# Performance work log

Hardware: AMD Instinct MI355X
Metric: run time of the kernel (lower is better)

## Reference

```python
import jax, jax.numpy as jnp
import numpy as np

NUM_ITERATIONS = 3  # matches init kwarg num_iterations
B, R, CIN, COUT, K = 32, 2048, 64, 64, 16


def squash(s):
    # squash along the last (capsule-vector) axis, as in the torch module
    sq = jnp.sum(s * s, axis=-1, keepdims=True)
    return (sq / (1.0 + sq)) * s / jnp.sqrt(sq)


def setup_inputs() -> dict:
    key = jax.random.key(0)
    k1, k2 = jax.random.split(key)
    x = jax.random.normal(k1, (B, R, CIN), dtype=jnp.float32)
    route_weights = jax.random.normal(k2, (K, R, CIN, COUT), dtype=jnp.float32) * 0.05
    return {"x": x, "route_weights": route_weights}


def reference(x, route_weights):
    # priors[k,b,r,o] = sum_c x[b,r,c] * W[k,r,c,o]   -> [K, B, R, COUT]
    priors = jnp.einsum('brc,krco->kbro', x, route_weights)
    logits = jnp.zeros(priors.shape[:3] + (1,), dtype=priors.dtype)  # [K,B,R,1]
    outputs = None
    for i in range(NUM_ITERATIONS):
        probs = jax.nn.softmax(logits, axis=2)  # softmax over route nodes (torch dim=2)
        outputs = squash(jnp.sum(probs * priors, axis=2, keepdims=True))  # [K,B,1,COUT]
        if i != NUM_ITERATIONS - 1:
            logits = logits + jnp.sum(priors * outputs, axis=-1, keepdims=True)
    return outputs[:, :, 0, :]  # [K, B, COUT]
```

## Files before the change

### kernel.cpp

```cpp
#include <hip/hip_runtime.h>
#include <hip/hip_bf16.h>
#include <stdint.h>

#define NB 32
#define NR 2048
#define NC 64
#define NO 64
#define NK 16

using bf16x8 = __attribute__((ext_vector_type(8))) short;
using f32x4  = __attribute__((ext_vector_type(4))) float;

__device__ __forceinline__ uint32_t f2bf(float f) {
  uint32_t u = __builtin_bit_cast(uint32_t, f);
  return (u + 0x7fffu + ((u >> 16) & 1u)) >> 16;
}
__device__ __forceinline__ uint32_t packbf2(float lo, float hi) {
  return f2bf(lo) | (f2bf(hi) << 16);
}
__device__ __forceinline__ uint32_t cvtpk2(float lo, float hi) {
  float2 v; v.x = lo; v.y = hi;
  __hip_bfloat162 h = __float22bfloat162_rn(v);
  uint32_t r;
  __builtin_memcpy(&r, &h, 4);
  return r;
}

__device__ __forceinline__ void gload_lds16(const float* g, float* l) {
  __builtin_amdgcn_global_load_lds(
      (const __attribute__((address_space(1))) void*)g,
      (__attribute__((address_space(3))) void*)l, 16, 0, 0);
}

__global__ __launch_bounds__(256) void make_xbf(const float* __restrict__ x,
                                                ushort* __restrict__ xbf) {
  __shared__ float tile[32][72];
  const int r = blockIdx.x, t = threadIdx.x;
  {
    const int b = t >> 3, c0 = (t & 7) << 3;
    const float* xp = x + ((size_t)b * NR + r) * NC + c0;
    *(float4*)&tile[b][c0] = *(const float4*)xp;
    *(float4*)&tile[b][c0 + 4] = *(const float4*)(xp + 4);
  }
  __syncthreads();
  {
    const int ks = t >> 7, mt = (t >> 6) & 1, l = t & 63;
    const int b = mt * 16 + (l & 15);
    const int cb = ks * 32 + (l >> 4) * 8;
    uint4 uv;
    uv.x = packbf2(tile[b][cb + 0], tile[b][cb + 1]);
    uv.y = packbf2(tile[b][cb + 2], tile[b][cb + 3]);
    uv.z = packbf2(tile[b][cb + 4], tile[b][cb + 5]);
    uv.w = packbf2(tile[b][cb + 6], tile[b][cb + 7]);
    *(uint4*)(xbf + (size_t)r * 2048 + t * 8) = uv;
  }
}

__global__ __launch_bounds__(256, 2) void priors_gemm(const ushort* __restrict__ xbf,
                                                      const float* __restrict__ W,
                                                      ushort* __restrict__ priors) {
  __shared__ float ldsW[2][4][2048];
  const int w = threadIdx.x >> 6, lane = threadIdx.x & 63;
  const int g = lane >> 4, col = lane & 15;
  const int kq = blockIdx.x & 3, rblk = blockIdx.x >> 2;
  const int k = kq * 4 + w;

  f32x4 acc[2][4];

  auto stage = [&](int rr, int ks, int buf) {
    const float* srcrow = W + ((size_t)(k * NR + rblk * 8 + rr)) * 4096 + ks * 2048;
    float* dst = &ldsW[buf][w][0] + lane * 4;
    const int j = lane & 15;
#pragma unroll
    for (int i = 0; i < 8; ++i) {
      const int c = i * 4 + (lane >> 4);
      const int gc = c >> 3;
      const int jj = j ^ (gc & 3) ^ ((gc >> 1) << 2);
      gload_lds16(srcrow + c * 64 + jj * 4, dst + i * 256);
    }
  };

  auto compute = [&](int rr, int ks, int buf) {
    const float* pw = &ldsW[buf][w][0];
    const size_t r = rblk * 8 + rr;
    bf16x8 af0 = *(const bf16x8*)(xbf + ((r * 2 + ks) * 2 + 0) * 512 + lane * 8);
    bf16x8 af1 = *(const bf16x8*)(xbf + ((r * 2 + ks) * 2 + 1) * 512 + lane * 8);
#pragma unroll
    for (int nt = 0; nt < 4; ++nt) {
      const int oo = (nt * 16 + col) ^ ((g & 3) << 2) ^ ((g >> 1) << 4);
      float f[8];
#pragma unroll
      for (int e = 0; e < 8; ++e) f[e] = pw[(g * 8 + e) * 64 + oo];
      uint4 uv;
      uv.x = cvtpk2(f[0], f[1]);
      uv.y = cvtpk2(f[2], f[3]);
      uv.z = cvtpk2(f[4], f[5]);
      uv.w = cvtpk2(f[6], f[7]);
      bf16x8 bfr = __builtin_bit_cast(bf16x8, uv);
      acc[0][nt] = __builtin_amdgcn_mfma_f32_16x16x32_bf16(af0, bfr, acc[0][nt], 0, 0, 0);
      acc[1][nt] = __builtin_amdgcn_mfma_f32_16x16x32_bf16(af1, bfr, acc[1][nt], 0, 0, 0);
    }
  };

  auto epilogue = [&](int rr, int buf) {
    ushort* ep = (ushort*)&ldsW[buf][w][0];
#pragma unroll
    for (int mt = 0; mt < 2; ++mt)
#pragma unroll
      for (int nt = 0; nt < 4; ++nt)
#pragma unroll
        for (int rp = 0; rp < 2; ++rp) {
          uint32_t u = cvtpk2(acc[mt][nt][rp * 2], acc[mt][nt][rp * 2 + 1]);
          const int row0 = mt * 16 + g * 4 + rp * 2;
          ep[(row0 + 0) * 64 + nt * 16 + col] = (ushort)u;
          ep[(row0 + 1) * 64 + nt * 16 + col] = (ushort)(u >> 16);
        }
    ushort* pp = priors + ((size_t)(k * NR + rblk * 8 + rr)) * 2048;
#pragma unroll
    for (int i = 0; i < 4; ++i) {
      uint4 v = *(const uint4*)(ep + lane * 8 + i * 512);
      *(uint4*)(pp + lane * 8 + i * 512) = v;
    }
  };

  stage(0, 0, 0);
  __syncthreads();
  for (int ti = 0; ti < 8; ++ti) {
#pragma unroll
    for (int mt = 0; mt < 2; ++mt)
#pragma unroll
      for (int nt = 0; nt < 4; ++nt) acc[mt][nt] = f32x4{0.f, 0.f, 0.f, 0.f};
    stage(ti, 1, 1);
    compute(ti, 0, 0);
    __syncthreads();
    if (ti < 7) stage(ti + 1, 0, 0);
    compute(ti, 1, 1);
    epilogue(ti, 1);
    __syncthreads();
  }
}

template <int PASS>
__global__ __launch_bounds__(256) void routing(const __hip_bfloat16* __restrict__ priors,
                                               float* __restrict__ Abuf,
                                               const float* __restrict__ o_prev,
                                               float* __restrict__ o_out) {
  __shared__ float o_lds[64];
  __shared__ float red_num[4][8][8];
  __shared__ float red_den[4];
  const int kb = blockIdx.x;
  const int k = kb >> 5, b = kb & 31;
  const int tid = threadIdx.x, w = tid >> 6, lane = tid & 63;
  const int g = lane >> 3, sl = lane & 7;
  const int rsub = w * 8 + g;
  const __hip_bfloat16* pbase = priors + (size_t)k * NR * NB * NO + (size_t)b * NO;
  float* ab = Abuf + (size_t)kb * NR;

  if (PASS == 1) {
    float sum[8];
#pragma unroll
    for (int j = 0; j < 8; ++j) sum[j] = 0.f;
    for (int it = 0; it < NR / 32; ++it) {
      const int r = it * 32 + rsub;
      uint4 pv = *(const uint4*)(pbase + (size_t)r * (NB * NO) + sl * 8);
      sum[0] += __builtin_bit_cast(float, pv.x << 16);
      sum[1] += __builtin_bit_cast(float, pv.x & 0xffff0000u);
      sum[2] += __builtin_bit_cast(float, pv.y << 16);
      sum[3] += __builtin_bit_cast(float, pv.y & 0xffff0000u);
      sum[4] += __builtin_bit_cast(float, pv.z << 16);
      sum[5] += __builtin_bit_cast(float, pv.z & 0xffff0000u);
      sum[6] += __builtin_bit_cast(float, pv.w << 16);
      sum[7] += __builtin_bit_cast(float, pv.w & 0xffff0000u);
    }
#pragma unroll
    for (int m = 8; m < 64; m <<= 1)
#pragma unroll
      for (int j = 0; j < 8; ++j) sum[j] += __shfl_xor(sum[j], m, 64);
    if (lane < 8) {
#pragma unroll
      for (int j = 0; j < 8; ++j) red_num[w][lane][j] = sum[j];
    }
    __syncthreads();
    if (tid < 64) {
      const int s_ = tid >> 3, j_ = tid & 7;
      float sv = (red_num[0][s_][j_] + red_num[1][s_][j_] +
                  red_num[2][s_][j_] + red_num[3][s_][j_]) * (1.f / (float)NR);
      float sq = sv * sv;
#pragma unroll
      for (int m = 1; m < 64; m <<= 1) sq += __shfl_xor(sq, m, 64);
      o_lds[tid] = (sq / (1.f + sq)) * rsqrtf(sq) * sv;
    }
    __syncthreads();
  } else {
    if (tid < 64) o_lds[tid] = o_prev[kb * 64 + tid];
    __syncthreads();
  }

  float os[8];
#pragma unroll
  for (int j = 0; j < 8; ++j) os[j] = o_lds[sl * 8 + j];

  float num[8];
#pragma unroll
  for (int j = 0; j < 8; ++j) num[j] = 0.f;
  float den = 0.f;

  for (int it = 0; it < NR / 32; ++it) {
    const int r = it * 32 + rsub;
    uint4 pv = *(const uint4*)(pbase + (size_t)r * (NB * NO) + sl * 8);
    float f[8];
    f[0] = __builtin_bit_cast(float, pv.x << 16);
    f[1] = __builtin_bit_cast(float, pv.x & 0xffff0000u);
    f[2] = __builtin_bit_cast(float, pv.y << 16);
    f[3] = __builtin_bit_cast(float, pv.y & 0xffff0000u);
    f[4] = __builtin_bit_cast(float, pv.z << 16);
    f[5] = __builtin_bit_cast(float, pv.z & 0xffff0000u);
    f[6] = __builtin_bit_cast(float, pv.w << 16);
    f[7] = __builtin_bit_cast(float, pv.w & 0xffff0000u);

    float d = 0.f;
#pragma unroll
    for (int j = 0; j < 8; ++j) d = fmaf(f[j], os[j], d);
#pragma unroll
    for (int m = 1; m < 8; m <<= 1) d += __shfl_xor(d, m, 64);

    float lg;
    if (PASS == 1) {
      lg = d;
      if (sl == 0) ab[r] = d;
    } else {
      lg = d + ab[r];
    }
    float e = __expf(lg);
    den += e;
#pragma unroll
    for (int j = 0; j < 8; ++j) num[j] = fmaf(e, f[j], num[j]);
  }

#pragma unroll
  for (int m = 8; m < 64; m <<= 1) {
    den += __shfl_xor(den, m, 64);
#pragma unroll
    for (int j = 0; j < 8; ++j) num[j] += __shfl_xor(num[j], m, 64);
  }
  if (lane < 8) {
#pragma unroll
    for (int j = 0; j < 8; ++j) red_num[w][lane][j] = num[j];
    if (lane == 0) red_den[w] = den;
  }
  __syncthreads();

  if (tid < 64) {
    const int s_ = tid >> 3, j_ = tid & 7;
    float nm = red_num[0][s_][j_] + red_num[1][s_][j_] + red_num[2][s_][j_] + red_num[3][s_][j_];
    float dn = red_den[0] + red_den[1] + red_den[2] + red_den[3];
    float sv = nm / dn;
    float sq = sv * sv;
#pragma unroll
    for (int m = 1; m < 64; m <<= 1) sq += __shfl_xor(sq, m, 64);
    float ov = (sq / (1.f + sq)) * rsqrtf(sq) * sv;
    o_out[kb * 64 + tid] = ov;
  }
}

extern "C" void kernel_launch(void* const* d_in, const int* in_sizes, int n_in,
                              void* d_out, int out_size, void* d_ws, size_t ws_size,
                              hipStream_t stream) {
  const float* x = (const float*)d_in[0];
  const float* W = (const float*)d_in[1];
  float* out = (float*)d_out;
  char* ws = (char*)d_ws;

  size_t off = 0;
  ushort* xbf = (ushort*)(ws + off);               off += (size_t)NR * 2048 * 2;
  ushort* priors = (ushort*)(ws + off);            off += (size_t)NK * NR * NB * NO * 2;
  float* o1 = (float*)(ws + off);                  off += (size_t)NK * NB * NO * 4;
  float* Abuf = (float*)(ws + off);                off += (size_t)NK * NB * NR * 4;

  make_xbf<<<NR, 256, 0, stream>>>(x, xbf);
  priors_gemm<<<(NR / 8) * (NK / 4), 256, 0, stream>>>(xbf, W, priors);
  routing<1><<<NK * NB, 256, 0, stream>>>((const __hip_bfloat16*)priors, Abuf, nullptr, o1);
  routing<2><<<NK * NB, 256, 0, stream>>>((const __hip_bfloat16*)priors, Abuf, o1, out);
}
```

Baseline: 241.4 us.

## Replace block barriers with vmcnt waits and separate epilogue LDS in priors GEMM

Removes the __syncthreads barriers in the priors GEMM loop. Each wave stages only its own slice of W in LDS, so it now waits on its own outstanding global-to-LDS loads with explicit s_waitcnt vmcnt counts. The x fragments for both k-halves are loaded up front. The epilogue gets a dedicated LDS buffer so it no longer overwrites the staging buffer. The cost is more shared memory per block, which may lower occupancy, and correctness now depends on hand-counted vmcnt values.

```diff
diff --git a/kernel.cpp b/kernel.cpp
--- a/kernel.cpp
+++ b/kernel.cpp
@@ -10,6 +10,9 @@
 
 using bf16x8 = __attribute__((ext_vector_type(8))) short;
 using f32x4  = __attribute__((ext_vector_type(4))) float;
+
+#define WAITVM(N) do { asm volatile("s_waitcnt vmcnt(" #N ")" ::: "memory"); \
+                       __builtin_amdgcn_sched_barrier(0); } while (0)
 
 __device__ __forceinline__ uint32_t f2bf(float f) {
   uint32_t u = __builtin_bit_cast(uint32_t, f);
@@ -60,6 +63,7 @@
                                                       const float* __restrict__ W,
                                                       ushort* __restrict__ priors) {
   __shared__ float ldsW[2][4][2048];
+  __shared__ ushort ldsE[4][2048];
   const int w = threadIdx.x >> 6, lane = threadIdx.x & 63;
   const int g = lane >> 4, col = lane & 15;
   const int kq = blockIdx.x & 3, rblk = blockIdx.x >> 2;
@@ -80,11 +84,8 @@
     }
   };
 
-  auto compute = [&](int rr, int ks, int buf) {
+  auto compute = [&](bf16x8 af0, bf16x8 af1, int buf) {
     const float* pw = &ldsW[buf][w][0];
-    const size_t r = rblk * 8 + rr;
-    bf16x8 af0 = *(const bf16x8*)(xbf + ((r * 2 + ks) * 2 + 0) * 512 + lane * 8);
-    bf16x8 af1 = *(const bf16x8*)(xbf + ((r * 2 + ks) * 2 + 1) * 512 + lane * 8);
 #pragma unroll
     for (int nt = 0; nt < 4; ++nt) {
       const int oo = (nt * 16 + col) ^ ((g & 3) << 2) ^ ((g >> 1) << 4);
@@ -102,8 +103,8 @@
     }
   };
 
-  auto epilogue = [&](int rr, int buf) {
-    ushort* ep = (ushort*)&ldsW[buf][w][0];
+  auto epilogue = [&](int rr) {
+    ushort* ep = &ldsE[w][0];
 #pragma unroll
     for (int mt = 0; mt < 2; ++mt)
 #pragma unroll
@@ -124,19 +125,27 @@
   };
 
   stage(0, 0, 0);
-  __syncthreads();
   for (int ti = 0; ti < 8; ++ti) {
+    const size_t r = rblk * 8 + ti;
+    bf16x8 a00 = *(const bf16x8*)(xbf + ((r * 2 + 0) * 2 + 0) * 512 + lane * 8);
+    bf16x8 a10 = *(const bf16x8*)(xbf + ((r * 2 + 0) * 2 + 1) * 512 + lane * 8);
+    bf16x8 a01 = *(const bf16x8*)(xbf + ((r * 2 + 1) * 2 + 0) * 512 + lane * 8);
+    bf16x8 a11 = *(const bf16x8*)(xbf + ((r * 2 + 1) * 2 + 1) * 512 + lane * 8);
+    stage(ti, 1, 1);
 #pragma unroll
     for (int mt = 0; mt < 2; ++mt)
 #pragma unroll
       for (int nt = 0; nt < 4; ++nt) acc[mt][nt] = f32x4{0.f, 0.f, 0.f, 0.f};
-    stage(ti, 1, 1);
-    compute(ti, 0, 0);
-    __syncthreads();
-    if (ti < 7) stage(ti + 1, 0, 0);
-    compute(ti, 1, 1);
-    epilogue(ti, 1);
-    __syncthreads();
+    WAITVM(12);
+    compute(a00, a10, 0);
+    if (ti < 7) {
+      stage(ti + 1, 0, 0);
+      WAITVM(8);
+    } else {
+      WAITVM(0);
+    }
+    compute(a01, a11, 1);
+    epilogue(ti);
   }
 }
 
```

After: 238.4 us. Within noise of the previous version (-1.2%).
